# Kernel tuning notes

Hardware: AMD Instinct MI355X
Metric: run time of the kernel (lower is better)

## Reference

```python
import jax, jax.numpy as jnp
import numpy as np

N, D, NUM_CLASSES = 1024, 256, 10
EPS = 1e-12


def setup_inputs() -> dict:
    key = jax.random.key(0)
    k1, k2, k3, k4 = jax.random.split(key, 4)
    return {
        "fm_s": jax.random.normal(k1, (N, D), dtype=jnp.float32),
        "fm_t": jax.random.normal(k2, (N, D), dtype=jnp.float32),
        "logvar_s": jax.random.normal(k3, (N, D), dtype=jnp.float32),
        "targets": jax.random.randint(k4, (N,), 0, NUM_CLASSES, dtype=jnp.int64),
        "fusion_true": 0,  # False branch (no multi_index)
    }


def reference(fm_s, fm_t, logvar_s, targets, fusion_true):
    # pairwise squared diff scaled by per-row (student) variance: (N, N, D)
    diff2 = (fm_s[:, None, :] - fm_t[None, :, :]) ** 2
    inv_var_term = diff2 / (2.0 * jnp.exp(logvar_s)[:, None, :] + EPS)
    half_lv = 0.5 * logvar_s[:, None, :]
    lp = jax.nn.relu(inv_var_term + half_lv).sum(-1)   # (N, N)
    ln = jax.nn.relu(-inv_var_term - half_lv).sum(-1)  # (N, N)
    pos = (targets[:, None] == targets[None, :]).astype(fm_s.dtype)  # self_mask_pos
    neg = 1.0 - pos
    loss_pos = lp * pos / pos.sum(-1, keepdims=True)
    loss_neg = ln * neg / neg.sum(-1, keepdims=True)
    # fusion_true == False path
    return loss_pos.sum(-1).mean() + loss_neg.sum(-1).mean()
```

## Files before the change

kernel.cpp:

```cpp
#include <hip/hip_runtime.h>
#include <math.h>

#define NN   1024
#define DD   256
#define NCLS 10

#define TI 64
#define TJ 128
#define DC 32
#define DSPLIT 8
#define NBLK ((NN / TI) * (NN / TJ) * DSPLIT)

typedef float f32x2 __attribute__((ext_vector_type(2)));
typedef float f32x4 __attribute__((ext_vector_type(4)));

#define PK_FMA(d, a, b, c) \
    asm("v_pk_fma_f32 %0, %1, %2, %3" : "=v"(d) : "v"(a), "v"(b), "v"(c))
#define PK_ADD(d, a, b) \
    asm("v_pk_add_f32 %0, %1, %2" : "=v"(d) : "v"(a), "v"(b))

__global__ __launch_bounds__(256) void count_kernel(const long long* __restrict__ tgt,
                                                    float* __restrict__ wtab) {
    __shared__ int c[NCLS];
    int tid = threadIdx.x;
    if (tid < NCLS) c[tid] = 0;
    __syncthreads();
    for (int k = tid; k < NN; k += 256) atomicAdd(&c[(int)tgt[k]], 1);
    __syncthreads();
    if (tid < NCLS) {
        wtab[tid]      = 1.0f / (float)c[tid];
        wtab[16 + tid] = 1.0f / (float)(NN - c[tid]);
    }
}

__global__ __launch_bounds__(256) void pair_kernel(
    const float* __restrict__ fm_s, const float* __restrict__ fm_t,
    const float* __restrict__ lv, const long long* __restrict__ tgt,
    const float* __restrict__ wtab, float* __restrict__ partials)
{
    __shared__ float Al[TI * DC];
    __shared__ float Bl[TI * DC];
    __shared__ float Vl[TI * DC];
    __shared__ float Fl[TJ * DC];

    const int bid  = blockIdx.x;
    const int tile = bid >> 3;
    const int kd   = bid & 7;
    const int i0   = (tile >> 3) * TI;
    const int j0   = (tile & 7) * TJ;
    const int doff = kd * DC;

    const int tid  = threadIdx.x;
    const int tx   = tid & 15;
    const int ty   = tid >> 4;
    const int lane = tid & 63;
    const int w    = tid >> 6;

    const int* tgt32 = (const int*)tgt;

    const int srow = tid >> 3;
    const int sq   = tid & 7;
#pragma unroll
    for (int p = 0; p < 4; ++p) {
        const int r = p * 32 + srow;
        f32x4 v = *(const f32x4*)&fm_t[(j0 + r) * DD + doff + sq * 4];
        const int phys = (sq + (r >> 3)) & 7;
        *(f32x4*)&Fl[r * DC + phys * 4] = v;
    }
#pragma unroll
    for (int p = 0; p < 2; ++p) {
        const int r = p * 32 + srow;
        const int g = (i0 + r) * DD + doff + sq * 4;
        f32x4 fs = *(const f32x4*)&fm_s[g];
        f32x4 l  = *(const f32x4*)&lv[g];
        f32x4 A, B, V;
#pragma unroll
        for (int e = 0; e < 4; ++e) {
            const float iv = 0.5f * __expf(-l[e]);
            const float fsiv = fs[e] * iv;
            A[e] = fmaf(fsiv, fs[e], 0.5f * l[e]);
            B[e] = -2.0f * fsiv;
            V[e] = iv;
        }
        const int phys = (sq + (r >> 2)) & 7;
        *(f32x4*)&Al[r * DC + phys * 4] = A;
        *(f32x4*)&Bl[r * DC + phys * 4] = B;
        *(f32x4*)&Vl[r * DC + phys * 4] = V;
    }

    __syncthreads();

    float s1[4][8], s2[4][8];
#pragma unroll
    for (int a = 0; a < 4; ++a)
#pragma unroll
        for (int b = 0; b < 8; ++b) { s1[a][b] = 0.f; s2[a][b] = 0.f; }

#pragma unroll
    for (int k = 0; k < 8; ++k) {
        const f32x4* pf = (const f32x4*)&Fl[tx * 256 + ((k + tx) & 7) * 4];
        f32x4 f[8];
#pragma unroll
        for (int rj = 0; rj < 8; ++rj) f[rj] = pf[rj * 8];

        const int iq = ((k + ty) & 7) * 4;
        const f32x4* pa = (const f32x4*)&Al[ty * 128 + iq];
        const f32x4* pb = (const f32x4*)&Bl[ty * 128 + iq];
        const f32x4* pv = (const f32x4*)&Vl[ty * 128 + iq];
#pragma unroll
        for (int ri = 0; ri < 4; ++ri) {
            const f32x4 fa = pa[ri * 8];
            const f32x4 fb = pb[ri * 8];
            const f32x4 fv = pv[ri * 8];
#pragma unroll
            for (int rj = 0; rj < 8; ++rj) {
                const f32x2 f01 = f[rj].lo, f23 = f[rj].hi;
                f32x2 u01, u23, t01, t23, st;
                PK_FMA(u01, fv.lo, f01, fb.lo);
                PK_FMA(u23, fv.hi, f23, fb.hi);
                PK_FMA(t01, u01, f01, fa.lo);
                PK_FMA(t23, u23, f23, fa.hi);
                PK_ADD(st, t01, t23);
                s1[ri][rj] += st.x + st.y;
                s2[ri][rj] += (fabsf(t01.x) + fabsf(t01.y))
                            + (fabsf(t23.x) + fabsf(t23.y));
            }
        }
    }

    float csum = 0.f;
#pragma unroll
    for (int ri = 0; ri < 4; ++ri) {
        const int t   = tgt32[(i0 + ty * 4 + ri) * 2];
        const float wp = wtab[t];
        const float wn = wtab[16 + t];
#pragma unroll
        for (int rj = 0; rj < 8; ++rj) {
            const int tj = tgt32[(j0 + tx * 8 + rj) * 2];
            const float lp = 0.5f * (s2[ri][rj] + s1[ri][rj]);
            const float ln = 0.5f * (s2[ri][rj] - s1[ri][rj]);
            csum += (t == tj) ? lp * wp : ln * wn;
        }
    }

#pragma unroll
    for (int off = 32; off > 0; off >>= 1) csum += __shfl_down(csum, off);
    __syncthreads();
    if (lane == 0) Al[w] = csum;
    __syncthreads();
    if (tid == 0) partials[bid] = (Al[0] + Al[1]) + (Al[2] + Al[3]);
}

__global__ __launch_bounds__(256) void finalize_kernel(const float* __restrict__ partials,
                                                       float* __restrict__ out) {
    __shared__ float red[256];
    const int tid = threadIdx.x;
    red[tid] = (partials[tid] + partials[tid + 256]) +
               (partials[tid + 512] + partials[tid + 768]);
    __syncthreads();
    for (int s = 128; s > 0; s >>= 1) {
        if (tid < s) red[tid] += red[tid + s];
        __syncthreads();
    }
    if (tid == 0) out[0] = red[0] * (1.0f / (float)NN);
}

extern "C" void kernel_launch(void* const* d_in, const int* in_sizes, int n_in,
                              void* d_out, int out_size, void* d_ws, size_t ws_size,
                              hipStream_t stream) {
    const float* fm_s    = (const float*)d_in[0];
    const float* fm_t    = (const float*)d_in[1];
    const float* lv      = (const float*)d_in[2];
    const long long* tgt = (const long long*)d_in[3];

    float* wtab     = (float*)d_ws;
    float* partials = (float*)((char*)d_ws + 256);

    hipLaunchKernelGGL(count_kernel, dim3(1), dim3(256), 0, stream, tgt, wtab);
    hipLaunchKernelGGL(pair_kernel, dim3(NBLK), dim3(256), 0, stream,
                       fm_s, fm_t, lv, tgt, wtab, partials);
    hipLaunchKernelGGL(finalize_kernel, dim3(1), dim3(256), 0, stream,
                       partials, (float*)d_out);
}
```

Measured before the change: 37.82 us.

## Halve j-tile to 64 and replace packed FMA asm with scalar FMA loops

Shrinks the j tile from 128 to 64 rows, doubling the block count to 2048 and cutting per-thread accumulators from 32 to 16 pairs. It also drops the inline v_pk_fma asm in favour of plain scalar fmaf loops with per-element abs accumulation. The finalize kernel is generalised to reduce the larger partials array. The aim is better occupancy and lower register pressure, at the cost of less reuse of the A/B/V tiles per block, more redundant exp work, and possibly losing packed-math throughput.

```diff
diff --git a/kernel.cpp b/kernel.cpp
--- a/kernel.cpp
+++ b/kernel.cpp
@@ -6,18 +6,12 @@
 #define NCLS 10
 
 #define TI 64
-#define TJ 128
+#define TJ 64
 #define DC 32
 #define DSPLIT 8
 #define NBLK ((NN / TI) * (NN / TJ) * DSPLIT)
 
-typedef float f32x2 __attribute__((ext_vector_type(2)));
 typedef float f32x4 __attribute__((ext_vector_type(4)));
-
-#define PK_FMA(d, a, b, c) \
-    asm("v_pk_fma_f32 %0, %1, %2, %3" : "=v"(d) : "v"(a), "v"(b), "v"(c))
-#define PK_ADD(d, a, b) \
-    asm("v_pk_add_f32 %0, %1, %2" : "=v"(d) : "v"(a), "v"(b))
 
 __global__ __launch_bounds__(256) void count_kernel(const long long* __restrict__ tgt,
                                                     float* __restrict__ wtab) {
@@ -46,8 +40,8 @@
     const int bid  = blockIdx.x;
     const int tile = bid >> 3;
     const int kd   = bid & 7;
-    const int i0   = (tile >> 3) * TI;
-    const int j0   = (tile & 7) * TJ;
+    const int i0   = (tile >> 4) * TI;
+    const int j0   = (tile & 15) * TJ;
     const int doff = kd * DC;
 
     const int tid  = threadIdx.x;
@@ -58,18 +52,14 @@
 
     const int* tgt32 = (const int*)tgt;
 
-    const int srow = tid >> 3;
-    const int sq   = tid & 7;
-#pragma unroll
-    for (int p = 0; p < 4; ++p) {
-        const int r = p * 32 + srow;
-        f32x4 v = *(const f32x4*)&fm_t[(j0 + r) * DD + doff + sq * 4];
-        const int phys = (sq + (r >> 3)) & 7;
-        *(f32x4*)&Fl[r * DC + phys * 4] = v;
-    }
+    const int sr = tid >> 3;
+    const int sq = tid & 7;
 #pragma unroll
     for (int p = 0; p < 2; ++p) {
-        const int r = p * 32 + srow;
+        const int r    = sr + p * 32;
+        const int phys = (sq + (r >> 2)) & 7;
+        f32x4 v = *(const f32x4*)&fm_t[(j0 + r) * DD + doff + sq * 4];
+        *(f32x4*)&Fl[r * DC + phys * 4] = v;
         const int g = (i0 + r) * DD + doff + sq * 4;
         f32x4 fs = *(const f32x4*)&fm_s[g];
         f32x4 l  = *(const f32x4*)&lv[g];
@@ -82,26 +72,26 @@
             B[e] = -2.0f * fsiv;
             V[e] = iv;
         }
-        const int phys = (sq + (r >> 2)) & 7;
-        *(f32x4*)&Al[r * DC + phys * 4] = A;
-        *(f32x4*)&Bl[r * DC + phys * 4] = B;
-        *(f32x4*)&Vl[r * DC + phys * 4] = V;
+        const int o = r * DC + phys * 4;
+        *(f32x4*)&Al[o] = A;
+        *(f32x4*)&Bl[o] = B;
+        *(f32x4*)&Vl[o] = V;
     }
 
     __syncthreads();
 
-    float s1[4][8], s2[4][8];
+    float s1[4][4], s2[4][4];
 #pragma unroll
     for (int a = 0; a < 4; ++a)
 #pragma unroll
-        for (int b = 0; b < 8; ++b) { s1[a][b] = 0.f; s2[a][b] = 0.f; }
+        for (int b = 0; b < 4; ++b) { s1[a][b] = 0.f; s2[a][b] = 0.f; }
 
+#pragma unroll 2
+    for (int k = 0; k < 8; ++k) {
+        const f32x4* pf = (const f32x4*)&Fl[tx * 128 + ((k + tx) & 7) * 4];
+        f32x4 f[4];
 #pragma unroll
-    for (int k = 0; k < 8; ++k) {
-        const f32x4* pf = (const f32x4*)&Fl[tx * 256 + ((k + tx) & 7) * 4];
-        f32x4 f[8];
-#pragma unroll
-        for (int rj = 0; rj < 8; ++rj) f[rj] = pf[rj * 8];
+        for (int rj = 0; rj < 4; ++rj) f[rj] = pf[rj * 8];
 
         const int iq = ((k + ty) & 7) * 4;
         const f32x4* pa = (const f32x4*)&Al[ty * 128 + iq];
@@ -113,17 +103,15 @@
             const f32x4 fb = pb[ri * 8];
             const f32x4 fv = pv[ri * 8];
 #pragma unroll
-            for (int rj = 0; rj < 8; ++rj) {
-                const f32x2 f01 = f[rj].lo, f23 = f[rj].hi;
-                f32x2 u01, u23, t01, t23, st;
-                PK_FMA(u01, fv.lo, f01, fb.lo);
-                PK_FMA(u23, fv.hi, f23, fb.hi);
-                PK_FMA(t01, u01, f01, fa.lo);
-                PK_FMA(t23, u23, f23, fa.hi);
-                PK_ADD(st, t01, t23);
-                s1[ri][rj] += st.x + st.y;
-                s2[ri][rj] += (fabsf(t01.x) + fabsf(t01.y))
-                            + (fabsf(t23.x) + fabsf(t23.y));
+            for (int rj = 0; rj < 4; ++rj) {
+#pragma unroll
+                for (int e = 0; e < 4; ++e) {
+                    const float fe = f[rj][e];
+                    const float u  = fmaf(fv[e], fe, fb[e]);
+                    const float t  = fmaf(u, fe, fa[e]);
+                    s1[ri][rj] += t;
+                    s2[ri][rj] += fabsf(t);
+                }
             }
         }
     }
@@ -131,12 +119,12 @@
     float csum = 0.f;
 #pragma unroll
     for (int ri = 0; ri < 4; ++ri) {
-        const int t   = tgt32[(i0 + ty * 4 + ri) * 2];
+        const int t    = tgt32[(i0 + ty * 4 + ri) * 2];
         const float wp = wtab[t];
         const float wn = wtab[16 + t];
 #pragma unroll
-        for (int rj = 0; rj < 8; ++rj) {
-            const int tj = tgt32[(j0 + tx * 8 + rj) * 2];
+        for (int rj = 0; rj < 4; ++rj) {
+            const int tj = tgt32[(j0 + tx * 4 + rj) * 2];
             const float lp = 0.5f * (s2[ri][rj] + s1[ri][rj]);
             const float ln = 0.5f * (s2[ri][rj] - s1[ri][rj]);
             csum += (t == tj) ? lp * wp : ln * wn;
@@ -155,11 +143,13 @@
                                                        float* __restrict__ out) {
     __shared__ float red[256];
     const int tid = threadIdx.x;
-    red[tid] = (partials[tid] + partials[tid + 256]) +
-               (partials[tid + 512] + partials[tid + 768]);
+    float s = 0.f;
+#pragma unroll
+    for (int k = 0; k < NBLK / 256; ++k) s += partials[tid + k * 256];
+    red[tid] = s;
     __syncthreads();
-    for (int s = 128; s > 0; s >>= 1) {
-        if (tid < s) red[tid] += red[tid + s];
+    for (int st = 128; st > 0; st >>= 1) {
+        if (tid < st) red[tid] += red[tid + st];
         __syncthreads();
     }
     if (tid == 0) out[0] = red[0] * (1.0f / (float)NN);
```

New measurement: 44.43 us. +17.5%, slower.
